# Performance work log

Measured on AMD Instinct MI355X. Metric: run time of the kernel, lower is better.

Reference implementation:

```python
import jax, jax.numpy as jnp
import numpy as np

TIME_CONSTANT = 1.0
VM_THRESHOLD = 2.0
WINDOW = 100          # integration_window
AMPLITUDE = 1.0


def setup_inputs() -> dict:
    key = jax.random.key(0)
    # [B, T, H, W, C] positive drive so integrate-and-fire actually spikes
    inputs = jax.random.uniform(key, (4, 200, 64, 64, 8), dtype=jnp.float32)
    return {"inputs": inputs}


def _process_chunk(chunk):
    """Iterative integrate-and-fire on one time chunk [B, T, H, W, C].
    Each while-iteration extracts one spike per neuron (first threshold
    crossing of the running cumsum), resets the membrane, and zeroes the
    consumed input so the next cumsum restarts after the spike."""
    B, T = chunk.shape[0], chunk.shape[1]
    img = chunk.shape[2:]
    spikes0 = jnp.zeros((B,) + img + (T + 1,), chunk.dtype)
    vout0 = jnp.zeros_like(chunk)

    def body(state):
        ch, vout, spikes, _ = state
        V = jnp.cumsum(ch * TIME_CONSTANT, axis=1)            # membrane potential
        temp = jax.nn.relu(V - VM_THRESHOLD)
        has = jnp.any(temp > 0)                                # any neuron fires?
        ctemp = jnp.cumsum(temp, axis=1)                       # zero before first crossing
        tstar = jnp.sum((ctemp == 0).astype(jnp.int32), axis=1)  # [B,H,W,C] spike time (T => none)
        spikes_new = spikes + jax.nn.one_hot(tstar, T + 1, dtype=ch.dtype)
        rolled = jnp.roll(ctemp, 1, axis=1).at[:, 0].set(0.0)  # nonzero strictly after spike
        mask = rolled == 0
        vout_spk = jnp.where(mask, vout + V, 0.0)              # record V up to spike, reset after
        ch_spk = jnp.where(mask, 0.0, ch)                      # consume input up to spike
        # if no spikes this pass: accumulate residual V and stop (do-while break)
        vout_n = jnp.where(has, vout_spk, vout + V)
        ch_n = jnp.where(has, ch_spk, ch)
        spikes_n = jnp.where(has, spikes_new, spikes)
        return ch_n, vout_n, spikes_n, jnp.logical_not(has)

    def cond(state):
        return jnp.logical_not(state[3])

    state = (chunk, vout0, spikes0, jnp.array(False))
    _, vout, spikes, _ = jax.lax.while_loop(cond, body, state)
    return vout, spikes[..., :T]   # drop the 'no spike' bin


def reference(inputs):
    T = inputs.shape[1]
    sizes = [WINDOW] * (T // WINDOW) + ([T % WINDOW] if T % WINDOW else [])
    spike_chunks = []
    start = 0
    for s in sizes:  # small fixed chunk loop (structural, not a data dim)
        ch = inputs[:, start:start + s]
        start += s
        _, sp = _process_chunk(ch)
        spike_chunks.append(sp)
    spikes = jnp.concatenate(spike_chunks, axis=-1)   # [B, H, W, C, T]
    out = jnp.swapaxes(spikes, 1, -1)                 # [B, T, W, C, H] (as in source)
    if AMPLITUDE != 1.0:
        out = out * AMPLITUDE
    return out
```

## Files before the change

### kernel.cpp

```cpp
#include <hip/hip_runtime.h>
#include <stdint.h>

#define BDIM   4
#define TTOT   200
#define CHUNK  100
#define HWC    32768
#define NREG   (BDIM * TTOT)
#define RS_WS  32768u
#define RS_IP  131072u

__global__ __launch_bounds__(256) void spike_kernel(const float* __restrict__ x,
                                                    uint8_t* __restrict__ spk,
                                                    unsigned rstride) {
    unsigned g     = blockIdx.x * 256u + threadIdx.x;
    unsigned chunk = g >> 16;
    unsigned p     = g & 65535u;
    unsigned b     = p >> 14;
    unsigned i     = (p & 16383u) * 2u;
    unsigned t0    = b * TTOT + chunk * CHUNK;

    const float2* xp = (const float2*)(x + (size_t)t0 * HWC + i);
    uint8_t*      sp = spk + (size_t)t0 * rstride + i;

    float a0 = 0.0f, a1 = 0.0f;
    for (int tb = 0; tb < CHUNK; tb += 4) {
        float2 v[4];
#pragma unroll
        for (int k = 0; k < 4; ++k) v[k] = xp[(size_t)k * (HWC / 2)];
        xp += 4 * (HWC / 2);
#pragma unroll
        for (int k = 0; k < 4; ++k) {
            a0 += v[k].x; a1 += v[k].y;
            unsigned s0 = 0u, s1 = 0u;
            if (a0 > 2.0f) { s0 = 1u; a0 = 0.0f; }
            if (a1 > 2.0f) { s1 = 1u; a1 = 0.0f; }
            *(uint16_t*)sp = (uint16_t)(s0 | (s1 << 8));
            sp += rstride;
        }
    }
}

__global__ __launch_bounds__(256) void transpose_ws(const uint8_t* __restrict__ spk,
                                                    float* __restrict__ out) {
    __shared__ uint32_t lds[64 * 65];
    unsigned blk = blockIdx.x;
    unsigned region = blk >> 1, half = blk & 1u;
    unsigned tid = threadIdx.x;

    const uint32_t* in32 = (const uint32_t*)(spk + (size_t)region * RS_WS);
#pragma unroll
    for (int it = 0; it < 16; ++it) {
        unsigned idx = it * 256u + tid;
        unsigned h = idx >> 6, wq = idx & 63u;
        lds[h * 65u + wq] = in32[h * 128u + half * 64u + wq];
    }
    __syncthreads();

    float4* out4 = (float4*)out + (size_t)region * 8192u + half * 4096u;
#pragma unroll
    for (int it = 0; it < 16; ++it) {
        unsigned f   = it * 256u + tid;
        unsigned wcl = f >> 4;
        unsigned h0  = (f & 15u) << 2;
        unsigned wq  = wcl >> 2, sel = (wcl & 3u) * 8u;
        float4 v;
        v.x = (float)((lds[(h0 + 0u) * 65u + wq] >> sel) & 1u);
        v.y = (float)((lds[(h0 + 1u) * 65u + wq] >> sel) & 1u);
        v.z = (float)((lds[(h0 + 2u) * 65u + wq] >> sel) & 1u);
        v.w = (float)((lds[(h0 + 3u) * 65u + wq] >> sel) & 1u);
        out4[f] = v;
    }
}

__global__ __launch_bounds__(512) void transpose_ip(float* __restrict__ out) {
    __shared__ uint32_t lds[64 * 129];
    unsigned region = blockIdx.x;
    unsigned tid = threadIdx.x;

    const uint32_t* in32 = (const uint32_t*)((const uint8_t*)out + (size_t)region * RS_IP);
#pragma unroll
    for (int it = 0; it < 16; ++it) {
        unsigned idx = it * 512u + tid;
        unsigned h = idx >> 7, wq = idx & 127u;
        lds[h * 129u + wq] = in32[idx];
    }
    __syncthreads();

    float4* out4 = (float4*)out + (size_t)region * 8192u;
#pragma unroll
    for (int it = 0; it < 16; ++it) {
        unsigned f  = it * 512u + tid;
        unsigned wc = f >> 4;
        unsigned h0 = (f & 15u) << 2;
        unsigned wq = wc >> 2, sel = (wc & 3u) * 8u;
        float4 v;
        v.x = (float)((lds[(h0 + 0u) * 129u + wq] >> sel) & 1u);
        v.y = (float)((lds[(h0 + 1u) * 129u + wq] >> sel) & 1u);
        v.z = (float)((lds[(h0 + 2u) * 129u + wq] >> sel) & 1u);
        v.w = (float)((lds[(h0 + 3u) * 129u + wq] >> sel) & 1u);
        out4[f] = v;
    }
}

extern "C" void kernel_launch(void* const* d_in, const int* in_sizes, int n_in,
                              void* d_out, int out_size, void* d_ws, size_t ws_size,
                              hipStream_t stream) {
    (void)in_sizes; (void)n_in; (void)out_size;
    const float* x = (const float*)d_in[0];
    float* out = (float*)d_out;

    const size_t spike_bytes = (size_t)NREG * RS_WS;
    if (ws_size >= spike_bytes) {
        uint8_t* spk = (uint8_t*)d_ws;
        hipLaunchKernelGGL(spike_kernel, dim3(512), dim3(256), 0, stream, x, spk, RS_WS);
        hipLaunchKernelGGL(transpose_ws, dim3(2 * NREG), dim3(256), 0, stream, spk, out);
    } else {
        hipLaunchKernelGGL(spike_kernel, dim3(512), dim3(256), 0, stream, x, (uint8_t*)out, RS_IP);
        hipLaunchKernelGGL(transpose_ip, dim3(NREG), dim3(512), 0, stream, out);
    }
}
```

Before: 188.2 us.

## Pack spikes as per-neuron bitmasks and expand with a tiled bit-transpose kernel

The spike pass now gives each thread one neuron and packs its 100 time steps into four 32-bit words, instead of writing one byte per time step into the workspace. The workspace shrinks from about 26 MB to 4 MB. A new expand kernel loads a tile of bit words into LDS and writes 25 time steps of float4 output per thread. This cuts intermediate memory traffic, at the cost of scalar per-thread input loads (no longer float2) and a heavier unrolled expand loop.

```diff
diff --git a/kernel.cpp b/kernel.cpp
--- a/kernel.cpp
+++ b/kernel.cpp
@@ -1,27 +1,126 @@
 #include <hip/hip_runtime.h>
 #include <stdint.h>
 
-#define BDIM   4
+#define HWC    32768
+#define NSLAB  8
 #define TTOT   200
 #define CHUNK  100
-#define HWC    32768
-#define NREG   (BDIM * TTOT)
-#define RS_WS  32768u
-#define RS_IP  131072u
 
-__global__ __launch_bounds__(256) void spike_kernel(const float* __restrict__ x,
-                                                    uint8_t* __restrict__ spk,
-                                                    unsigned rstride) {
+__global__ __launch_bounds__(256) void spike_bits(const float* __restrict__ x,
+                                                  uint32_t* __restrict__ spk) {
+    unsigned g    = blockIdx.x * 256u + threadIdx.x;
+    unsigned slab = g >> 15;
+    unsigned n    = g & (HWC - 1);
+    unsigned b    = slab >> 1, ch = slab & 1u;
+    const float* xp = x + (size_t)(b * TTOT + ch * CHUNK) * HWC + n;
+
+    float acc = 0.0f;
+    uint32_t w0 = 0u, w1 = 0u, w2 = 0u, w3 = 0u;
+    uint32_t* wsel[1]; (void)wsel;
+
+#define STEP(WREG, TB, K)                                         \
+    do {                                                          \
+        acc += v[K];                                              \
+        if (acc > 2.0f) { WREG |= (1u << ((TB) + (K))); acc = 0.0f; } \
+    } while (0)
+
+#define GROUP8(WREG, TBASE)                                       \
+    do {                                                          \
+        float v[8];                                               \
+        _Pragma("unroll")                                         \
+        for (int k = 0; k < 8; ++k) v[k] = xp[(size_t)((TBASE) + k) * HWC]; \
+        STEP(WREG, (TBASE) & 31, 0); STEP(WREG, (TBASE) & 31, 1); \
+        STEP(WREG, (TBASE) & 31, 2); STEP(WREG, (TBASE) & 31, 3); \
+        STEP(WREG, (TBASE) & 31, 4); STEP(WREG, (TBASE) & 31, 5); \
+        STEP(WREG, (TBASE) & 31, 6); STEP(WREG, (TBASE) & 31, 7); \
+    } while (0)
+
+    GROUP8(w0,  0); GROUP8(w0,  8); GROUP8(w0, 16); GROUP8(w0, 24);
+    GROUP8(w1, 32); GROUP8(w1, 40); GROUP8(w1, 48); GROUP8(w1, 56);
+    GROUP8(w2, 64); GROUP8(w2, 72); GROUP8(w2, 80); GROUP8(w2, 88);
+    {
+        float v[4];
+#pragma unroll
+        for (int k = 0; k < 4; ++k) v[k] = xp[(size_t)(96 + k) * HWC];
+        STEP(w3, 0, 0); STEP(w3, 0, 1); STEP(w3, 0, 2); STEP(w3, 0, 3);
+    }
+#undef GROUP8
+#undef STEP
+
+    uint32_t* sp = spk + ((size_t)slab << 17);
+    sp[n]            = w0;
+    sp[HWC + n]      = w1;
+    sp[2u * HWC + n] = w2;
+    sp[3u * HWC + n] = w3;
+}
+
+__global__ __launch_bounds__(512) void expand_bits(const uint32_t* __restrict__ spk,
+                                                   float* __restrict__ out) {
+    __shared__ uint32_t lds[2 * 2112];
+    unsigned gid  = blockIdx.x;
+    unsigned slab = gid >> 6;
+    unsigned q    = (gid >> 4) & 3u;
+    unsigned tile = gid & 15u;
+    unsigned wc0  = tile * 32u;
+    unsigned t0   = q * 25u;
+    unsigned p0   = t0 >> 5;
+    unsigned p1   = (t0 + 24u) >> 5;
+    unsigned tid  = threadIdx.x;
+
+    const uint32_t* sbase = spk + ((size_t)slab << 17);
+#pragma unroll
+    for (int it = 0; it < 8; ++it) {
+        unsigned idx = it * 512u + tid;
+        unsigned pl  = idx >> 11;
+        unsigned r   = idx & 2047u;
+        unsigned h   = r >> 5, wcl = r & 31u;
+        unsigned tw  = pl ? p1 : p0;
+        lds[pl * 2112u + h * 33u + wcl] =
+            sbase[((size_t)tw << 15) + h * 512u + wc0 + wcl];
+    }
+    __syncthreads();
+
+    unsigned wcl = tid >> 4;
+    unsigned h0  = (tid & 15u) * 4u;
+    uint32_t r0[4], r1[4];
+#pragma unroll
+    for (int k = 0; k < 4; ++k) {
+        r0[k] = lds[(h0 + k) * 33u + wcl];
+        r1[k] = lds[2112u + (h0 + k) * 33u + wcl];
+    }
+
+    unsigned b = slab >> 1, ch = slab & 1u;
+    unsigned rbase = b * TTOT + ch * CHUNK;
+    float4* o4 = (float4*)out;
+
+#pragma unroll
+    for (int j = 0; j < 25; ++j) {
+        unsigned t   = t0 + j;
+        unsigned sel = (t >> 5) != p0;
+        unsigned bit = t & 31u;
+        uint32_t a0 = sel ? r1[0] : r0[0];
+        uint32_t a1 = sel ? r1[1] : r0[1];
+        uint32_t a2 = sel ? r1[2] : r0[2];
+        uint32_t a3 = sel ? r1[3] : r0[3];
+        float4 v;
+        v.x = (float)((a0 >> bit) & 1u);
+        v.y = (float)((a1 >> bit) & 1u);
+        v.z = (float)((a2 >> bit) & 1u);
+        v.w = (float)((a3 >> bit) & 1u);
+        o4[(size_t)(rbase + t) * 8192u + wc0 * 16u + tid] = v;
+    }
+}
+
+__global__ __launch_bounds__(256) void spike_kernel_ip(const float* __restrict__ x,
+                                                       uint8_t* __restrict__ spk) {
     unsigned g     = blockIdx.x * 256u + threadIdx.x;
     unsigned chunk = g >> 16;
     unsigned p     = g & 65535u;
     unsigned b     = p >> 14;
     unsigned i     = (p & 16383u) * 2u;
     unsigned t0    = b * TTOT + chunk * CHUNK;
-
     const float2* xp = (const float2*)(x + (size_t)t0 * HWC + i);
-    uint8_t*      sp = spk + (size_t)t0 * rstride + i;
-
+    uint8_t*      sp = spk + (size_t)t0 * 131072u + i;
     float a0 = 0.0f, a1 = 0.0f;
     for (int tb = 0; tb < CHUNK; tb += 4) {
         float2 v[4];
@@ -35,40 +134,8 @@
             if (a0 > 2.0f) { s0 = 1u; a0 = 0.0f; }
             if (a1 > 2.0f) { s1 = 1u; a1 = 0.0f; }
             *(uint16_t*)sp = (uint16_t)(s0 | (s1 << 8));
-            sp += rstride;
+            sp += 131072u;
         }
-    }
-}
-
-__global__ __launch_bounds__(256) void transpose_ws(const uint8_t* __restrict__ spk,
-                                                    float* __restrict__ out) {
-    __shared__ uint32_t lds[64 * 65];
-    unsigned blk = blockIdx.x;
-    unsigned region = blk >> 1, half = blk & 1u;
-    unsigned tid = threadIdx.x;
-
-    const uint32_t* in32 = (const uint32_t*)(spk + (size_t)region * RS_WS);
-#pragma unroll
-    for (int it = 0; it < 16; ++it) {
-        unsigned idx = it * 256u + tid;
-        unsigned h = idx >> 6, wq = idx & 63u;
-        lds[h * 65u + wq] = in32[h * 128u + half * 64u + wq];
-    }
-    __syncthreads();
-
-    float4* out4 = (float4*)out + (size_t)region * 8192u + half * 4096u;
-#pragma unroll
-    for (int it = 0; it < 16; ++it) {
-        unsigned f   = it * 256u + tid;
-        unsigned wcl = f >> 4;
-        unsigned h0  = (f & 15u) << 2;
-        unsigned wq  = wcl >> 2, sel = (wcl & 3u) * 8u;
-        float4 v;
-        v.x = (float)((lds[(h0 + 0u) * 65u + wq] >> sel) & 1u);
-        v.y = (float)((lds[(h0 + 1u) * 65u + wq] >> sel) & 1u);
-        v.z = (float)((lds[(h0 + 2u) * 65u + wq] >> sel) & 1u);
-        v.w = (float)((lds[(h0 + 3u) * 65u + wq] >> sel) & 1u);
-        out4[f] = v;
     }
 }
 
@@ -76,8 +143,7 @@
     __shared__ uint32_t lds[64 * 129];
     unsigned region = blockIdx.x;
     unsigned tid = threadIdx.x;
-
-    const uint32_t* in32 = (const uint32_t*)((const uint8_t*)out + (size_t)region * RS_IP);
+    const uint32_t* in32 = (const uint32_t*)((const uint8_t*)out + (size_t)region * 131072u);
 #pragma unroll
     for (int it = 0; it < 16; ++it) {
         unsigned idx = it * 512u + tid;
@@ -85,7 +151,6 @@
         lds[h * 129u + wq] = in32[idx];
     }
     __syncthreads();
-
     float4* out4 = (float4*)out + (size_t)region * 8192u;
 #pragma unroll
     for (int it = 0; it < 16; ++it) {
@@ -109,13 +174,13 @@
     const float* x = (const float*)d_in[0];
     float* out = (float*)d_out;
 
-    const size_t spike_bytes = (size_t)NREG * RS_WS;
-    if (ws_size >= spike_bytes) {
-        uint8_t* spk = (uint8_t*)d_ws;
-        hipLaunchKernelGGL(spike_kernel, dim3(512), dim3(256), 0, stream, x, spk, RS_WS);
-        hipLaunchKernelGGL(transpose_ws, dim3(2 * NREG), dim3(256), 0, stream, spk, out);
+    const size_t bit_bytes = (size_t)NSLAB * 4u * HWC * 4u;
+    if (ws_size >= bit_bytes) {
+        uint32_t* spk = (uint32_t*)d_ws;
+        hipLaunchKernelGGL(spike_bits, dim3(1024), dim3(256), 0, stream, x, spk);
+        hipLaunchKernelGGL(expand_bits, dim3(512), dim3(512), 0, stream, spk, out);
     } else {
-        hipLaunchKernelGGL(spike_kernel, dim3(512), dim3(256), 0, stream, x, (uint8_t*)out, RS_IP);
-        hipLaunchKernelGGL(transpose_ip, dim3(NREG), dim3(512), 0, stream, out);
+        hipLaunchKernelGGL(spike_kernel_ip, dim3(512), dim3(256), 0, stream, x, (uint8_t*)out);
+        hipLaunchKernelGGL(transpose_ip, dim3(NSLAB * CHUNK), dim3(512), 0, stream, out);
     }
 }
```

Result: faster. 182.0 us (-3.3%).
